# Performance work log

Measured on AMD Instinct MI355X. Metric: run time of the kernel, lower is better.

Reference implementation:

```python
import jax, jax.numpy as jnp
import numpy as np

L, D, H, HD, M = 4096, 1024, 16, 64, 4096
EPS = 1e-5


def setup_inputs() -> dict:
    key = jax.random.key(0)
    ks = jax.random.split(key, 12)
    hidden_states = jax.random.normal(ks[0], (L, D), dtype=jnp.float32)
    cu_seqlens = jnp.arange(5, dtype=jnp.int32) * (L // 4)  # [0,1024,2048,3072,4096]
    # rope freqs as cos/sin of random angles: (L, HD//2, 2)
    angles = jax.random.uniform(ks[1], (L, HD // 2), dtype=jnp.float32) * (2.0 * np.pi)
    rope_freqs = jnp.stack([jnp.cos(angles), jnp.sin(angles)], axis=-1)
    s = 0.02
    params = {
        "ln0_g": jnp.ones((D,), jnp.float32), "ln0_b": jnp.zeros((D,), jnp.float32),
        "ln1_g": jnp.ones((D,), jnp.float32), "ln1_b": jnp.zeros((D,), jnp.float32),
        "w_qkv": jax.random.normal(ks[2], (D, 3 * D), jnp.float32) * s,
        "w_o":   jax.random.normal(ks[3], (D, D), jnp.float32) * s,
        "w_fc0": jax.random.normal(ks[4], (D, M), jnp.float32) * s,
        "b_fc0": jnp.zeros((M,), jnp.float32),
        "w_fc1": jax.random.normal(ks[5], (M, D), jnp.float32) * s,
        "b_fc1": jnp.zeros((D,), jnp.float32),
    }
    return {"hidden_states": hidden_states, "cu_seqlens": cu_seqlens, "rope_freqs": rope_freqs, **params}


def _layernorm(x, g, b):
    mu = jnp.mean(x, axis=-1, keepdims=True)
    var = jnp.var(x, axis=-1, keepdims=True)
    return (x - mu) * jax.lax.rsqrt(var + EPS) * g + b


def _apply_rope(x, fc):
    # x: (L, H, HD); fc: (L, HD//2, 2) -> broadcast over heads
    xr = x.reshape(L, H, HD // 2, 2)
    a, b = xr[..., 0], xr[..., 1]
    c, s = fc[:, None, :, 0], fc[:, None, :, 1]
    out = jnp.stack([a * c - b * s, a * s + b * c], axis=-1)
    return out.reshape(L, H, HD)


def reference(hidden_states, cu_seqlens, rope_freqs, ln0_g, ln0_b, ln1_g, ln1_b,
              w_qkv, w_o, w_fc0, b_fc0, w_fc1, b_fc1):
    residual = hidden_states
    x = _layernorm(hidden_states, ln0_g, ln0_b)
    qkv = (x @ w_qkv).reshape(L, 3, H, HD)
    q, k, v = qkv[:, 0], qkv[:, 1], qkv[:, 2]
    q = _apply_rope(q, rope_freqs)
    k = _apply_rope(k, rope_freqs)
    # block-diagonal mask from cu_seqlens
    seg = jnp.searchsorted(cu_seqlens[1:], jnp.arange(L, dtype=cu_seqlens.dtype), side="right")
    mask = seg[:, None] == seg[None, :]  # (L, L)
    scale = 1.0 / np.sqrt(HD)
    scores = jnp.einsum("lhd,mhd->hlm", q, k) * scale
    scores = jnp.where(mask[None], scores, jnp.float32(-1e30))
    probs = jax.nn.softmax(scores, axis=-1)
    attn = jnp.einsum("hlm,mhd->lhd", probs, v).reshape(L, D)
    attn = attn @ w_o
    h = residual + attn
    y = _layernorm(h, ln1_g, ln1_b)
    y = jax.nn.gelu(y @ w_fc0 + b_fc0, approximate=False) @ w_fc1 + b_fc1
    return h + y
```

## Files before the change

kernel.cpp:

```cpp
#include <hip/hip_runtime.h>
#include <cstdint>
#include <cmath>

#define L_ 4096
#define D_ 1024
#define H_ 16
#define HD_ 64
#define M_ 4096

typedef __bf16 bf16_t;
typedef __attribute__((ext_vector_type(8))) __bf16 bf16x8;
typedef __attribute__((ext_vector_type(4))) __bf16 bf16x4;
typedef __attribute__((ext_vector_type(4))) float f32x4;

#define WAIT_VM0 0x0f70
#define WAIT_LGKM0 0xc07f

__device__ __forceinline__ f32x4 mfma16(bf16x8 a, bf16x8 b, f32x4 c) {
    return __builtin_amdgcn_mfma_f32_16x16x32_bf16(a, b, c, 0, 0, 0);
}

__device__ __forceinline__ void gload_lds16(const bf16_t* g, bf16_t* l) {
    __builtin_amdgcn_global_load_lds(
        (const __attribute__((address_space(1))) unsigned int*)(g),
        (__attribute__((address_space(3))) unsigned int*)(l), 16, 0, 0);
}

__device__ __forceinline__ float fast_exp2(float x) {
    float r;
    asm volatile("v_exp_f32 %0, %1" : "=v"(r) : "v"(x));
    return r;
}
__device__ __forceinline__ float fast_rcp(float x) {
    float r;
    asm volatile("v_rcp_f32 %0, %1" : "=v"(r) : "v"(x));
    return r;
}
__device__ __forceinline__ float gelu_f(float v) {
    float t = v * (0.7978845608f + 0.0356774081f * v * v);
    return v * fast_rcp(1.f + fast_exp2(-2.885390082f * t));
}

__global__ __launch_bounds__(256) void ln_kernel(const float* __restrict__ x,
                                                 const float* __restrict__ g,
                                                 const float* __restrict__ b,
                                                 bf16_t* __restrict__ out) {
    int row = blockIdx.x, tid = threadIdx.x;
    int wave = tid >> 6, lane = tid & 63;
    const f32x4* xr = (const f32x4*)(x + (long)row * D_);
    f32x4 v = xr[tid];
    float s = v.x + v.y + v.z + v.w;
    __shared__ float red[8];
#pragma unroll
    for (int off = 32; off > 0; off >>= 1) s += __shfl_down(s, off, 64);
    if (lane == 0) red[wave] = s;
    __syncthreads();
    float mean = (red[0] + red[1] + red[2] + red[3]) * (1.f / 1024.f);
    float s2 = 0.f;
#pragma unroll
    for (int i = 0; i < 4; i++) { float d = v[i] - mean; s2 += d * d; }
#pragma unroll
    for (int off = 32; off > 0; off >>= 1) s2 += __shfl_down(s2, off, 64);
    __syncthreads();
    if (lane == 0) red[wave] = s2;
    __syncthreads();
    float var = (red[0] + red[1] + red[2] + red[3]) * (1.f / 1024.f);
    float rstd = rsqrtf(var + 1e-5f);
    f32x4 g4 = ((const f32x4*)g)[tid];
    f32x4 b4 = ((const f32x4*)b)[tid];
    bf16x4 o;
#pragma unroll
    for (int i = 0; i < 4; i++) o[i] = (bf16_t)((v[i] - mean) * rstd * g4[i] + b4[i]);
    *(bf16x4*)(out + (long)row * D_ + tid * 4) = o;
}

__global__ __launch_bounds__(256) void transpose_all(
    const float* __restrict__ w_qkv, const float* __restrict__ w_o,
    const float* __restrict__ w_fc0, const float* __restrict__ w_fc1,
    bf16_t* __restrict__ t_qkv, bf16_t* __restrict__ t_o,
    bf16_t* __restrict__ t_fc0, bf16_t* __restrict__ t_fc1) {
    __shared__ float t[32][33];
    int bidx = blockIdx.x;
    const float* W;
    bf16_t* Wt;
    int K, N, tile;
    if (bidx < 3072) { W = w_qkv; Wt = t_qkv; K = 1024; N = 3072; tile = bidx; }
    else if (bidx < 4096) { W = w_o; Wt = t_o; K = 1024; N = 1024; tile = bidx - 3072; }
    else if (bidx < 8192) { W = w_fc0; Wt = t_fc0; K = 1024; N = 4096; tile = bidx - 4096; }
    else { W = w_fc1; Wt = t_fc1; K = 4096; N = 1024; tile = bidx - 8192; }
    int nt = N >> 5;
    int n0 = (tile % nt) * 32, k0 = (tile / nt) * 32;
    int tx = threadIdx.x & 31, ty = threadIdx.x >> 5;
#pragma unroll
    for (int r = 0; r < 32; r += 8)
        t[ty + r][tx] = W[(long)(k0 + ty + r) * N + n0 + tx];
    __syncthreads();
#pragma unroll
    for (int r = 0; r < 32; r += 8)
        Wt[(long)(n0 + ty + r) * K + k0 + tx] = (bf16_t)t[tx][ty + r];
}

__global__ __launch_bounds__(256) void vt_kernel(const bf16_t* __restrict__ qkv,
                                                 bf16_t* __restrict__ Vt) {
    __shared__ bf16_t t[32][33];
    int l0 = blockIdx.x * 32, c0 = blockIdx.y * 32;
    int tx = threadIdx.x & 31, ty = threadIdx.x >> 5;
#pragma unroll
    for (int r = 0; r < 32; r += 8)
        t[ty + r][tx] = qkv[(long)(l0 + ty + r) * 3072 + 2048 + c0 + tx];
    __syncthreads();
#pragma unroll
    for (int r = 0; r < 32; r += 8)
        Vt[(long)(c0 + ty + r) * 4096 + l0 + tx] = t[tx][ty + r];
}

__global__ __launch_bounds__(256) void rope_kernel(bf16_t* __restrict__ qkv,
                                                   const float* __restrict__ freqs) {
    const float k1 = 0.125f * 1.44269504089f;
    int idx = blockIdx.x * 256 + threadIdx.x;
    int g = idx & 7;
    int h = (idx >> 3) & 15;
    int l = idx >> 7;
    const float* f = freqs + (long)l * 64 + g * 8;
    f32x4 f0 = ((const f32x4*)f)[0];
    f32x4 f1 = ((const f32x4*)f)[1];
    float c[4] = {f0.x, f0.z, f1.x, f1.z};
    float s[4] = {f0.y, f0.w, f1.y, f1.w};
    bf16_t* qp = qkv + (long)l * 3072 + h * 64 + g * 8;
    bf16x8 q = *(bf16x8*)qp;
    bf16x8 k = *(bf16x8*)(qp + 1024);
    bf16x8 qo, ko;
#pragma unroll
    for (int e = 0; e < 4; e++) {
        float a = (float)q[2 * e], b = (float)q[2 * e + 1];
        qo[2 * e] = (bf16_t)((a * c[e] - b * s[e]) * k1);
        qo[2 * e + 1] = (bf16_t)((a * s[e] + b * c[e]) * k1);
        a = (float)k[2 * e]; b = (float)k[2 * e + 1];
        ko[2 * e] = (bf16_t)(a * c[e] - b * s[e]);
        ko[2 * e + 1] = (bf16_t)(a * s[e] + b * c[e]);
    }
    *(bf16x8*)qp = qo;
    *(bf16x8*)(qp + 1024) = ko;
}

#define STAGE_A(d, h, kt)                                                          \
    gload_lds16(aSt + (long)((h) * 128) * K + (kt), &SA[d][h][(wv * 16) * 64]);    \
    gload_lds16(aSt + (long)((h) * 128 + 8) * K + (kt), &SA[d][h][(wv * 16 + 8) * 64]);

#define STAGE_B(d, h, kt)                                                          \
    gload_lds16(bSt + (long)((h) * 128) * K + (kt), &SB[d][h][(wv * 16) * 64]);    \
    gload_lds16(bSt + (long)((h) * 128 + 8) * K + (kt), &SB[d][h][(wv * 16 + 8) * 64]);

#define RD_A(dst, src, rq)                                                          \
    _Pragma("unroll") for (int i_ = 0; i_ < 4; i_++) {                              \
        dst[i_][0] = *(const bf16x8*)&src[((rq) * 64 + i_ * 16 + l16) * 64 + sl0 * 8]; \
        dst[i_][1] = *(const bf16x8*)&src[((rq) * 64 + i_ * 16 + l16) * 64 + sl1 * 8]; \
    }

#define RD_B(dst, src, cq)                                                          \
    _Pragma("unroll") for (int j_ = 0; j_ < 2; j_++) {                              \
        dst[j_][0] = *(const bf16x8*)&src[(bro + (cq) * 32 + j_ * 16 + l16) * 64 + sl0 * 8]; \
        dst[j_][1] = *(const bf16x8*)&src[(bro + (cq) * 32 + j_ * 16 + l16) * 64 + sl1 * 8]; \
    }

#define MFMA_Q(rq, cq, Af, Bf)                                                      \
    _Pragma("unroll") for (int i_ = 0; i_ < 4; i_++)                                \
    _Pragma("unroll") for (int j_ = 0; j_ < 2; j_++) {                              \
        acc[(rq) * 4 + i_][(cq) * 2 + j_] =                                         \
            mfma16(Af[i_][0], Bf[j_][0], acc[(rq) * 4 + i_][(cq) * 2 + j_]);        \
        acc[(rq) * 4 + i_][(cq) * 2 + j_] =                                         \
            mfma16(Af[i_][1], Bf[j_][1], acc[(rq) * 4 + i_][(cq) * 2 + j_]);        \
    }

#define LGKM0() asm volatile("s_waitcnt lgkmcnt(0)" ::: "memory")
#define VMC(n) asm volatile("s_waitcnt vmcnt(" #n ")" ::: "memory")
#define BAR() __builtin_amdgcn_s_barrier()
#define PRIO1() __builtin_amdgcn_s_setprio(1)
#define PRIO0() __builtin_amdgcn_s_setprio(0)

template <int EPI>
__device__ __forceinline__ void gemm256_core(
    const bf16_t* __restrict__ A, const bf16_t* __restrict__ Bt,
    int K, int N, long bm, long bn, int kb, int ke,
    bf16_t* __restrict__ outB, const float* __restrict__ bias) {
    __shared__ __align__(16) bf16_t SA[2][2][128 * 64];
    __shared__ __align__(16) bf16_t SB[2][2][128 * 64];
    int tid = threadIdx.x;
    int wv = tid >> 6, lane = tid & 63;
    int quad = lane >> 4, l16 = lane & 15;
    int wm = wv >> 2, wn = wv & 3;
    int lr = lane >> 3;
    int sc = (lane & 7) ^ (lr & 7);
    int sl0 = quad ^ (l16 & 7);
    int sl1 = (4 + quad) ^ (l16 & 7);
    int bro = (wn & 1) * 64;

    const bf16_t* aSt = A + (bm + wv * 16 + lr) * (long)K + sc * 8;
    const bf16_t* bSt = Bt + (bn + wv * 16 + lr) * (long)K + sc * 8;
    const bf16_t* pa0 = SA[0][wm];
    const bf16_t* pa1 = SA[1][wm];
    const bf16_t* pb0 = SB[0][wn >> 1];
    const bf16_t* pb1 = SB[1][wn >> 1];

    f32x4 acc[8][4];
#pragma unroll
    for (int i = 0; i < 8; i++)
#pragma unroll
        for (int j = 0; j < 4; j++) acc[i][j] = (f32x4){0.f, 0.f, 0.f, 0.f};

    bf16x8 a0[4][2], a1[4][2], b0[2][2], b1[2][2];

    STAGE_B(0, 0, kb); STAGE_B(0, 1, kb); STAGE_A(0, 0, kb); STAGE_A(0, 1, kb);
    STAGE_B(1, 0, kb + 64); STAGE_B(1, 1, kb + 64);
    STAGE_A(1, 0, kb + 64); STAGE_A(1, 1, kb + 64);
    VMC(8);
    BAR();
    RD_A(a0, pa0, 0); RD_B(b0, pb0, 0); RD_B(b1, pb0, 1);
    LGKM0();

    for (int k0 = kb; k0 < ke; k0 += 128) {
        int kt2 = (k0 + 128 < ke) ? k0 + 128 : kb;
        int kt3 = kt2 + 64;
        BAR(); STAGE_B(0, 0, kt2); STAGE_B(0, 1, kt2);
        PRIO1(); MFMA_Q(0, 0, a0, b0); MFMA_Q(0, 1, a0, b1); PRIO0();
        RD_A(a1, pa0, 1); LGKM0();
        VMC(4);
        BAR(); STAGE_A(0, 0, kt2); STAGE_A(0, 1, kt2);
        PRIO1(); MFMA_Q(1, 0, a1, b0); MFMA_Q(1, 1, a1, b1); PRIO0();
        RD_A(a0, pa1, 0); RD_B(b0, pb1, 0); RD_B(b1, pb1, 1); LGKM0();
        BAR(); STAGE_B(1, 0, kt3); STAGE_B(1, 1, kt3);
        PRIO1(); MFMA_Q(0, 0, a0, b0); MFMA_Q(0, 1, a0, b1); PRIO0();
        RD_A(a1, pa1, 1); LGKM0();
        VMC(4);
        BAR(); STAGE_A(1, 0, kt3); STAGE_A(1, 1, kt3);
        PRIO1(); MFMA_Q(1, 0, a1, b0); MFMA_Q(1, 1, a1, b1); PRIO0();
        RD_A(a0, pa0, 0); RD_B(b0, pb0, 0); RD_B(b1, pb0, 1); LGKM0();
    }
    VMC(0);

#pragma unroll
    for (int ri = 0; ri < 8; ri++)
#pragma unroll
        for (int cj = 0; cj < 4; cj++)
#pragma unroll
            for (int r = 0; r < 4; r++) {
                long row = bm + wm * 128 + (ri >> 2) * 64 + (ri & 3) * 16 + quad * 4 + r;
                long col = bn + wn * 64 + (cj >> 1) * 32 + (cj & 1) * 16 + l16;
                long idx = row * (long)N + col;
                float v = acc[ri][cj][r];
                if (EPI == 0) {
                    outB[idx] = (bf16_t)v;
                } else {
                    v += bias[col];
                    outB[idx] = (bf16_t)gelu_f(v);
                }
            }
}

__global__ __launch_bounds__(512) void gemm256_qkv(const bf16_t* __restrict__ A,
                                                   const bf16_t* __restrict__ Bt,
                                                   bf16_t* __restrict__ outB) {
    int g = blockIdx.x & 7, w = blockIdx.x >> 3;
    int gm = g >> 2, gn = g & 3;
    long bm = (long)(gm * 8 + w / 3) * 256;
    long bn = (long)(gn * 3 + w % 3) * 256;
    gemm256_core<0>(A, Bt, 1024, 3072, bm, bn, 0, 1024, outB, nullptr);
}

__global__ __launch_bounds__(512) void gemm256_fc0(const bf16_t* __restrict__ A,
                                                   const bf16_t* __restrict__ Bt,
                                                   bf16_t* __restrict__ outB,
                                                   const float* __restrict__ bias) {
    int g = blockIdx.x & 7, w = blockIdx.x >> 3;
    int gm = g >> 2, gn = g & 3;
    long bm = (long)(gm * 8 + (w >> 2)) * 256;
    long bn = (long)(gn * 4 + (w & 3)) * 256;
    gemm256_core<2>(A, Bt, 1024, 4096, bm, bn, 0, 1024, outB, bias);
}

__global__ __launch_bounds__(512) void gemm256_fc1(const bf16_t* __restrict__ A,
                                                   const bf16_t* __restrict__ Bt,
                                                   bf16_t* __restrict__ P) {
    int g = blockIdx.x & 7, w = blockIdx.x >> 3;
    int z = g >> 1, gm = g & 1;
    long bm = (long)(gm * 8 + (w >> 2)) * 256;
    long bn = (long)(w & 3) * 256;
    gemm256_core<0>(A, Bt, 4096, 1024, bm, bn, z * 1024, z * 1024 + 1024,
                    P + (long)z * L_ * D_, nullptr);
}

__global__ __launch_bounds__(256) void reduce_fc1(const bf16_t* __restrict__ P,
                                                  const float* __restrict__ bias,
                                                  float* __restrict__ out) {
    long i = (long)blockIdx.x * 256 + threadIdx.x;
    f32x4 b = ((const f32x4*)bias)[i & 255];
    f32x4 v = ((f32x4*)out)[i];
#pragma unroll
    for (int z = 0; z < 4; z++) {
        bf16x4 p = ((const bf16x4*)(P + (long)z * L_ * D_))[i];
#pragma unroll
        for (int e = 0; e < 4; e++) v[e] += (float)p[e];
    }
    v.x += b.x; v.y += b.y; v.z += b.z; v.w += b.w;
    ((f32x4*)out)[i] = v;
}

__global__ __launch_bounds__(256) void gemm_bt64_res(const bf16_t* __restrict__ A,
                                                     const bf16_t* __restrict__ Bt,
                                                     int M, int N, int K,
                                                     float* __restrict__ outF,
                                                     const float* __restrict__ res) {
    __shared__ __align__(16) bf16_t As[128 * 64];
    __shared__ __align__(16) bf16_t Bs[64 * 64];
    int tid = threadIdx.x;
    int wave = tid >> 6, lane = tid & 63;
    int quad = lane >> 4, l16 = lane & 15;

    int g = blockIdx.x & 7, w = blockIdx.x >> 3;
    int bn_i = w & 15, bm_i = g * 4 + (w >> 4);
    long bm = (long)bm_i * 128, bn = (long)bn_i * 64;

    f32x4 acc[2][4];
#pragma unroll
    for (int i = 0; i < 2; i++)
#pragma unroll
        for (int j = 0; j < 4; j++) acc[i][j] = (f32x4){0.f, 0.f, 0.f, 0.f};

    int lr = lane >> 3;
    int sc = (lane & 7) ^ (lr & 7);
    const bf16_t* a_base = A + (bm + wave * 32 + lr) * (long)K + sc * 8;
    const bf16_t* b_base = Bt + (bn + wave * 16 + lr) * (long)K + sc * 8;

    for (int k0 = 0; k0 < K; k0 += 64) {
        __syncthreads();
#pragma unroll
        for (int i = 0; i < 4; i++)
            gload_lds16(a_base + k0 + (long)(8 * i) * K, &As[(wave * 32 + 8 * i) * 64]);
#pragma unroll
        for (int i = 0; i < 2; i++)
            gload_lds16(b_base + k0 + (long)(8 * i) * K, &Bs[(wave * 16 + 8 * i) * 64]);
        __builtin_amdgcn_s_waitcnt(WAIT_VM0);
        __syncthreads();

#pragma unroll
        for (int h = 0; h < 2; h++) {
            int sl = (h * 4 + quad) ^ (l16 & 7);
            bf16x8 af[2], bfr[4];
#pragma unroll
            for (int i = 0; i < 2; i++)
                af[i] = *(const bf16x8*)&As[(wave * 32 + i * 16 + l16) * 64 + sl * 8];
#pragma unroll
            for (int j = 0; j < 4; j++)
                bfr[j] = *(const bf16x8*)&Bs[(j * 16 + l16) * 64 + sl * 8];
#pragma unroll
            for (int i = 0; i < 2; i++)
#pragma unroll
                for (int j = 0; j < 4; j++)
                    acc[i][j] = mfma16(af[i], bfr[j], acc[i][j]);
        }
    }

#pragma unroll
    for (int i = 0; i < 2; i++)
#pragma unroll
        for (int j = 0; j < 4; j++)
#pragma unroll
            for (int r = 0; r < 4; r++) {
                long row = bm + wave * 32 + i * 16 + quad * 4 + r;
                long col = bn + j * 16 + l16;
                long idx = row * (long)N + col;
                outF[idx] = acc[i][j][r] + res[idx];
            }
}

__global__ __launch_bounds__(256) void attn_kernel(const bf16_t* __restrict__ qkv,
                                                   const bf16_t* __restrict__ Vt,
                                                   const int* __restrict__ cu,
                                                   bf16_t* __restrict__ out) {
    __shared__ __align__(16) bf16_t QPs[4 * 16 * 72];
    __shared__ __align__(16) bf16_t Ks[2][64 * 64];
    __shared__ __align__(16) bf16_t Vs[2][64 * 64];

    int tid = threadIdx.x, wave = tid >> 6, lane = tid & 63;
    int quad = lane >> 4, l16 = lane & 15;

    int g = blockIdx.x & 7, w = blockIdx.x >> 3;
    int head = (w & 1) * 8 + g;
    int qt = (w >> 1) & 15;
    int seg = w >> 5;
    int s0 = cu[seg], s1 = cu[seg + 1];
    int r0 = s0 + qt * 64;
    const long hoff = (long)head * 64;

    bf16_t* Qs = QPs;
    bf16_t* Psw = &QPs[wave * 16 * 72];

    int lr = lane >> 3;
    int sc = (lane & 7) ^ (lr & 7);
    int sl0 = (0 * 4 + quad) ^ (l16 & 7);
    int sl1 = (1 * 4 + quad) ^ (l16 & 7);

#pragma unroll
    for (int i = 0; i < 2; i++) {
        int row = wave * 16 + i * 8 + lr;
        gload_lds16(qkv + (long)(r0 + row) * 3072 + hoff + sc * 8,
                    &Qs[(wave * 16 + i * 8) * 64]);
    }
    __builtin_amdgcn_s_waitcnt(WAIT_VM0);
    __syncthreads();
    bf16x8 aq0 = *(const bf16x8*)&Qs[(wave * 16 + l16) * 64 + sl0 * 8];
    bf16x8 aq1 = *(const bf16x8*)&Qs[(wave * 16 + l16) * 64 + sl1 * 8];

    bf16x8 ones;
#pragma unroll
    for (int e = 0; e < 8; e++) ones[e] = (bf16_t)1.0f;

    f32x4 o[4];
#pragma unroll
    for (int j = 0; j < 4; j++) o[j] = (f32x4){0.f, 0.f, 0.f, 0.f};
    f32x4 lacc = (f32x4){0.f, 0.f, 0.f, 0.f};

    for (int kt = s0; kt < s1; kt += 128) {
        __syncthreads();
#pragma unroll
        for (int i = 0; i < 2; i++) {
            int row = wave * 16 + i * 8 + lr;
            long kr0 = (long)(kt + row) * 3072 + 1024 + hoff + sc * 8;
            gload_lds16(qkv + kr0, &Ks[0][(wave * 16 + i * 8) * 64]);
            gload_lds16(qkv + kr0 + (long)64 * 3072, &Ks[1][(wave * 16 + i * 8) * 64]);
            long vr0 = (hoff + row) * (long)4096 + kt + sc * 8;
            gload_lds16(Vt + vr0, &Vs[0][(wave * 16 + i * 8) * 64]);
            gload_lds16(Vt + vr0 + 64, &Vs[1][(wave * 16 + i * 8) * 64]);
        }
        __builtin_amdgcn_s_waitcnt(WAIT_VM0);
        __syncthreads();

#pragma unroll
        for (int half = 0; half < 2; half++) {
            f32x4 sacc[4];
#pragma unroll
            for (int j = 0; j < 4; j++) sacc[j] = (f32x4){0.f, 0.f, 0.f, 0.f};
#pragma unroll
            for (int j = 0; j < 4; j++) {
                bf16x8 b0 = *(const bf16x8*)&Ks[half][(j * 16 + l16) * 64 + sl0 * 8];
                bf16x8 b1 = *(const bf16x8*)&Ks[half][(j * 16 + l16) * 64 + sl1 * 8];
                sacc[j] = mfma16(aq0, b0, sacc[j]);
                sacc[j] = mfma16(aq1, b1, sacc[j]);
            }

#pragma unroll
            for (int j = 0; j < 4; j++)
#pragma unroll
                for (int r = 0; r < 4; r++)
                    Psw[(quad * 4 + r) * 72 + j * 16 + l16] = (bf16_t)fast_exp2(sacc[j][r]);

            __builtin_amdgcn_s_waitcnt(WAIT_LGKM0);

            bf16x8 ap0 = *(const bf16x8*)&Psw[l16 * 72 + 0 * 32 + quad * 8];
            bf16x8 ap1 = *(const bf16x8*)&Psw[l16 * 72 + 1 * 32 + quad * 8];
#pragma unroll
            for (int j2 = 0; j2 < 4; j2++) {
                bf16x8 b0 = *(const bf16x8*)&Vs[half][(j2 * 16 + l16) * 64 + sl0 * 8];
                bf16x8 b1 = *(const bf16x8*)&Vs[half][(j2 * 16 + l16) * 64 + sl1 * 8];
                o[j2] = mfma16(ap0, b0, o[j2]);
                o[j2] = mfma16(ap1, b1, o[j2]);
            }
            lacc = mfma16(ap0, ones, lacc);
            lacc = mfma16(ap1, ones, lacc);
        }
    }

#pragma unroll
    for (int r = 0; r < 4; r++) {
        float inv = fast_rcp(lacc[r]);
        int row = r0 + wave * 16 + quad * 4 + r;
#pragma unroll
        for (int j2 = 0; j2 < 4; j2++)
            out[(long)row * 1024 + head * 64 + j2 * 16 + l16] = (bf16_t)(o[j2][r] * inv);
    }
}

extern "C" void kernel_launch(void* const* d_in, const int* in_sizes, int n_in,
                              void* d_out, int out_size, void* d_ws, size_t ws_size,
                              hipStream_t stream) {
    const float* hidden = (const float*)d_in[0];
    const int* cu = (const int*)d_in[1];
    const float* freqs = (const float*)d_in[2];
    const float* ln0_g = (const float*)d_in[3];
    const float* ln0_b = (const float*)d_in[4];
    const float* ln1_g = (const float*)d_in[5];
    const float* ln1_b = (const float*)d_in[6];
    const float* w_qkv = (const float*)d_in[7];
    const float* w_o = (const float*)d_in[8];
    const float* w_fc0 = (const float*)d_in[9];
    const float* b_fc0 = (const float*)d_in[10];
    const float* w_fc1 = (const float*)d_in[11];
    const float* b_fc1 = (const float*)d_in[12];
    float* out = (float*)d_out;

    char* ws = (char*)d_ws;
    bf16_t* qkv = (bf16_t*)(ws);
    bf16_t* attn = (bf16_t*)(ws + ((size_t)24 << 20));
    bf16_t* act = (bf16_t*)(ws);
    bf16_t* x_bf = (bf16_t*)(ws + ((size_t)32 << 20));
    bf16_t* Vt = x_bf;
    bf16_t* y_bf = x_bf;
    bf16_t* fc1p = (bf16_t*)(ws + ((size_t)40 << 20));
    bf16_t* wqkvT = (bf16_t*)(ws + ((size_t)72 << 20));
    bf16_t* woT = (bf16_t*)(ws + ((size_t)78 << 20));
    bf16_t* wfc0T = (bf16_t*)(ws + ((size_t)80 << 20));
    bf16_t* wfc1T = (bf16_t*)(ws + ((size_t)88 << 20));
    float* h = out;

    transpose_all<<<12288, 256, 0, stream>>>(w_qkv, w_o, w_fc0, w_fc1,
                                             wqkvT, woT, wfc0T, wfc1T);

    ln_kernel<<<L_, 256, 0, stream>>>(hidden, ln0_g, ln0_b, x_bf);

    gemm256_qkv<<<192, 512, 0, stream>>>(x_bf, wqkvT, qkv);

    rope_kernel<<<(L_ * H_ * 8) / 256, 256, 0, stream>>>(qkv, freqs);
    vt_kernel<<<dim3(4096 / 32, 1024 / 32), 256, 0, stream>>>(qkv, Vt);

    attn_kernel<<<1024, 256, 0, stream>>>(qkv, Vt, cu, attn);

    gemm_bt64_res<<<512, 256, 0, stream>>>(
        attn, woT, L_, 1024, 1024, h, hidden);

    ln_kernel<<<L_, 256, 0, stream>>>(h, ln1_g, ln1_b, y_bf);

    gemm256_fc0<<<256, 512, 0, stream>>>(y_bf, wfc0T, act, b_fc0);

    gemm256_fc1<<<256, 512, 0, stream>>>(act, wfc1T, fc1p);
    reduce_fc1<<<(L_ * D_ / 4) / 256, 256, 0, stream>>>(fc1p, b_fc1, out);
}
```

Measured before the change: 311.2 us.

## Double-buffer K/V tiles in attention loop with async prefetch two tiles ahead

Restructures the attention inner loop from loading 128-key blocks synchronously into two LDS halves into a 64-key ring of two buffers. The tile two steps ahead is prefetched with global_load_lds while the current tile is computed, using partial vmcnt waits instead of draining all loads each iteration. This is meant to hide global memory latency behind MFMA work. It adds an extra barrier per tile and issues redundant loads on the final iterations.

```diff
diff --git a/kernel.cpp b/kernel.cpp
--- a/kernel.cpp
+++ b/kernel.cpp
@@ -406,8 +406,20 @@
         gload_lds16(qkv + (long)(r0 + row) * 3072 + hoff + sc * 8,
                     &Qs[(wave * 16 + i * 8) * 64]);
     }
-    __builtin_amdgcn_s_waitcnt(WAIT_VM0);
-    __syncthreads();
+#pragma unroll
+    for (int tp = 0; tp < 2; tp++) {
+#pragma unroll
+        for (int i = 0; i < 2; i++) {
+            int row = wave * 16 + i * 8 + lr;
+            long kt = s0 + tp * 64;
+            gload_lds16(qkv + (kt + row) * (long)3072 + 1024 + hoff + sc * 8,
+                        &Ks[tp][(wave * 16 + i * 8) * 64]);
+            gload_lds16(Vt + (hoff + row) * (long)4096 + kt + sc * 8,
+                        &Vs[tp][(wave * 16 + i * 8) * 64]);
+        }
+    }
+    VMC(8);
+    BAR();
     bf16x8 aq0 = *(const bf16x8*)&Qs[(wave * 16 + l16) * 64 + sl0 * 8];
     bf16x8 aq1 = *(const bf16x8*)&Qs[(wave * 16 + l16) * 64 + sl1 * 8];
 
@@ -420,55 +432,56 @@
     for (int j = 0; j < 4; j++) o[j] = (f32x4){0.f, 0.f, 0.f, 0.f};
     f32x4 lacc = (f32x4){0.f, 0.f, 0.f, 0.f};
 
-    for (int kt = s0; kt < s1; kt += 128) {
-        __syncthreads();
+    int nt = (s1 - s0) >> 6;
+    for (int t = 0; t < nt; t++) {
+        int cur = t & 1;
+        VMC(4);
+        BAR();
+
+        f32x4 sacc[4];
+#pragma unroll
+        for (int j = 0; j < 4; j++) sacc[j] = (f32x4){0.f, 0.f, 0.f, 0.f};
+#pragma unroll
+        for (int j = 0; j < 4; j++) {
+            bf16x8 b0 = *(const bf16x8*)&Ks[cur][(j * 16 + l16) * 64 + sl0 * 8];
+            bf16x8 b1 = *(const bf16x8*)&Ks[cur][(j * 16 + l16) * 64 + sl1 * 8];
+            sacc[j] = mfma16(aq0, b0, sacc[j]);
+            sacc[j] = mfma16(aq1, b1, sacc[j]);
+        }
+
+#pragma unroll
+        for (int j = 0; j < 4; j++)
+#pragma unroll
+            for (int r = 0; r < 4; r++)
+                Psw[(quad * 4 + r) * 72 + j * 16 + l16] = (bf16_t)fast_exp2(sacc[j][r]);
+
+        __builtin_amdgcn_s_waitcnt(WAIT_LGKM0);
+
+        bf16x8 ap0 = *(const bf16x8*)&Psw[l16 * 72 + 0 * 32 + quad * 8];
+        bf16x8 ap1 = *(const bf16x8*)&Psw[l16 * 72 + 1 * 32 + quad * 8];
+#pragma unroll
+        for (int j2 = 0; j2 < 4; j2++) {
+            bf16x8 b0 = *(const bf16x8*)&Vs[cur][(j2 * 16 + l16) * 64 + sl0 * 8];
+            bf16x8 b1 = *(const bf16x8*)&Vs[cur][(j2 * 16 + l16) * 64 + sl1 * 8];
+            o[j2] = mfma16(ap0, b0, o[j2]);
+            o[j2] = mfma16(ap1, b1, o[j2]);
+        }
+        lacc = mfma16(ap0, ones, lacc);
+        lacc = mfma16(ap1, ones, lacc);
+
+        BAR();
+        int t2 = (t + 2 < nt) ? t + 2 : t;
+        long kt2 = s0 + (long)t2 * 64;
 #pragma unroll
         for (int i = 0; i < 2; i++) {
             int row = wave * 16 + i * 8 + lr;
-            long kr0 = (long)(kt + row) * 3072 + 1024 + hoff + sc * 8;
-            gload_lds16(qkv + kr0, &Ks[0][(wave * 16 + i * 8) * 64]);
-            gload_lds16(qkv + kr0 + (long)64 * 3072, &Ks[1][(wave * 16 + i * 8) * 64]);
-            long vr0 = (hoff + row) * (long)4096 + kt + sc * 8;
-            gload_lds16(Vt + vr0, &Vs[0][(wave * 16 + i * 8) * 64]);
-            gload_lds16(Vt + vr0 + 64, &Vs[1][(wave * 16 + i * 8) * 64]);
+            gload_lds16(qkv + (kt2 + row) * (long)3072 + 1024 + hoff + sc * 8,
+                        &Ks[cur][(wave * 16 + i * 8) * 64]);
+            gload_lds16(Vt + (hoff + row) * (long)4096 + kt2 + sc * 8,
+                        &Vs[cur][(wave * 16 + i * 8) * 64]);
         }
-        __builtin_amdgcn_s_waitcnt(WAIT_VM0);
-        __syncthreads();
-
-#pragma unroll
-        for (int half = 0; half < 2; half++) {
-            f32x4 sacc[4];
-#pragma unroll
-            for (int j = 0; j < 4; j++) sacc[j] = (f32x4){0.f, 0.f, 0.f, 0.f};
-#pragma unroll
-            for (int j = 0; j < 4; j++) {
-                bf16x8 b0 = *(const bf16x8*)&Ks[half][(j * 16 + l16) * 64 + sl0 * 8];
-                bf16x8 b1 = *(const bf16x8*)&Ks[half][(j * 16 + l16) * 64 + sl1 * 8];
-                sacc[j] = mfma16(aq0, b0, sacc[j]);
-                sacc[j] = mfma16(aq1, b1, sacc[j]);
-            }
-
-#pragma unroll
-            for (int j = 0; j < 4; j++)
-#pragma unroll
-                for (int r = 0; r < 4; r++)
-                    Psw[(quad * 4 + r) * 72 + j * 16 + l16] = (bf16_t)fast_exp2(sacc[j][r]);
-
-            __builtin_amdgcn_s_waitcnt(WAIT_LGKM0);
-
-            bf16x8 ap0 = *(const bf16x8*)&Psw[l16 * 72 + 0 * 32 + quad * 8];
-            bf16x8 ap1 = *(const bf16x8*)&Psw[l16 * 72 + 1 * 32 + quad * 8];
-#pragma unroll
-            for (int j2 = 0; j2 < 4; j2++) {
-                bf16x8 b0 = *(const bf16x8*)&Vs[half][(j2 * 16 + l16) * 64 + sl0 * 8];
-                bf16x8 b1 = *(const bf16x8*)&Vs[half][(j2 * 16 + l16) * 64 + sl1 * 8];
-                o[j2] = mfma16(ap0, b0, o[j2]);
-                o[j2] = mfma16(ap1, b1, o[j2]);
-            }
-            lacc = mfma16(ap0, ones, lacc);
-            lacc = mfma16(ap1, ones, lacc);
-        }
-    }
+    }
+    VMC(0);
 
 #pragma unroll
     for (int r = 0; r < 4; r++) {
```

Measured after the change: 315.0 us. No clear change (+1.2%).
